# Kernel tuning notes

Hardware: AMD Instinct MI355X
Metric: run time of the kernel (lower is better)

## Reference

```python
import jax, jax.numpy as jnp
import numpy as np

N_NODES = 100000
N_EDGES = 1600000
ATOM_EMB = 64
BOND_EMB = 16
MSG_DIM = 64
OUT_HIDDEN = 128
N_MOLS = 2048
MSG_PASSES = 4


def setup_inputs() -> dict:
    key = jax.random.key(0)
    ks = jax.random.split(key, 16)
    x = jax.random.randint(ks[0], (N_NODES,), 0, 119)
    edge_attr = jax.random.randint(ks[1], (N_EDGES,), 0, 4)
    edge_index = jax.random.randint(ks[2], (2, N_EDGES), 0, N_NODES)
    batch = jnp.sort(jax.random.randint(ks[3], (N_NODES,), 0, N_MOLS))
    s = 0.02
    atom_table = jax.random.normal(ks[4], (119, ATOM_EMB), jnp.float32) * s
    bond_table = jax.random.normal(ks[5], (4, BOND_EMB), jnp.float32) * s
    Wi = jax.random.normal(ks[6], (ATOM_EMB + BOND_EMB, MSG_DIM), jnp.float32) * s
    bi = jnp.zeros((MSG_DIM,), jnp.float32)
    Wu = jax.random.normal(ks[7], (ATOM_EMB + BOND_EMB + MSG_DIM, MSG_DIM), jnp.float32) * s
    bu = jnp.zeros((MSG_DIM,), jnp.float32)
    W1 = jax.random.normal(ks[8], (MSG_DIM, OUT_HIDDEN), jnp.float32) * s
    b1 = jnp.zeros((OUT_HIDDEN,), jnp.float32)
    W2 = jax.random.normal(ks[9], (OUT_HIDDEN, 1), jnp.float32) * s
    b2 = jnp.zeros((1,), jnp.float32)
    return {"x": x, "edge_attr": edge_attr, "edge_index": edge_index, "batch": batch,
            "atom_table": atom_table, "bond_table": bond_table,
            "Wi": Wi, "bi": bi, "Wu": Wu, "bu": bu,
            "W1": W1, "b1": b1, "W2": W2, "b2": b2}


def reference(x, edge_attr, edge_index, batch, atom_table, bond_table, Wi, bi, Wu, bu, W1, b1, W2, b2):
    atom = atom_table[x]                      # [N, ATOM_EMB]
    bond = bond_table[edge_attr]              # [E, BOND_EMB]
    src, dst = edge_index[0], edge_index[1]
    atom_src = atom[src]                      # [E, ATOM_EMB]
    ab = jnp.concatenate([atom_src, bond], axis=1)
    msg = jax.nn.relu(ab @ Wi + bi)           # [E, MSG_DIM]
    for _ in range(MSG_PASSES):
        agg = jax.ops.segment_sum(msg, dst, num_segments=N_NODES)  # [N, MSG_DIM]
        upd_in = jnp.concatenate([ab, agg[src]], axis=1)           # [E, 144]
        msg = jax.nn.relu(upd_in @ Wu + bu)
    node_state = jax.ops.segment_sum(msg, dst, num_segments=N_NODES)
    mol_state = jax.ops.segment_sum(node_state, batch, num_segments=N_MOLS)
    h = jax.nn.relu(mol_state @ W1 + b1)
    return (h @ W2 + b2).squeeze(-1)          # [N_MOLS]
```

## Files before the change

### kernel.cpp

```cpp
#include <hip/hip_runtime.h>

#define MSG 64
#define SLICE_SHIFT 9
#define SLICE_N (1 << SLICE_SHIFT)
#define MAXSLICES 256
#define REP 8
#define CAP_R 1536
#define CAP_E 12288
#define CAP_B 16384
#define NBIN 64

typedef _Float16 h2 __attribute__((ext_vector_type(2)));
typedef _Float16 h4 __attribute__((ext_vector_type(4)));
typedef _Float16 h8 __attribute__((ext_vector_type(8)));

__device__ inline h8 relu8(h8 v) {
    h8 z = {};
    return __builtin_elementwise_max(v, z);
}

__device__ inline h2 u2h(unsigned u) { union { unsigned u; h2 h; } c; c.u = u; return c.h; }

__global__ void setup_kernel(const float* __restrict__ atom, const float* __restrict__ bond,
                             const float* __restrict__ Wi, const float* __restrict__ bi,
                             const float* __restrict__ Wu, const float* __restrict__ bu,
                             const float* __restrict__ Wagg,
                             _Float16* __restrict__ tAi, _Float16* __restrict__ tBi,
                             _Float16* __restrict__ tAu, _Float16* __restrict__ tBu,
                             unsigned* __restrict__ wst, int* __restrict__ gcur,
                             int* __restrict__ bcnt, float* __restrict__ mol,
                             int AR, int K, int ab) {
    int b = blockIdx.x;
    if (b < 2 * ab + 2) {
        bool upd = b >= ab + 1;
        const float* W = upd ? Wu : Wi;
        int lb = upd ? b - (ab + 1) : b;
        if (lb < ab) {
            _Float16* tA = upd ? tAu : tAi;
            int t = lb * 256 + threadIdx.x;
            if (t < AR * MSG) {
                int i = t & 63, a = t >> 6;
                float s = 0.f;
                for (int k = 0; k < 64; ++k) s = fmaf(atom[a * 64 + k], W[k * 64 + i], s);
                tA[t] = (_Float16)s;
            }
        } else {
            _Float16* tBo = upd ? tBu : tBi;
            const float* bias = upd ? bu : bi;
            const float* W16 = W + 64 * MSG;
            int t = threadIdx.x;
            int i = t & 63, r = t >> 6;
            float s = bias[i];
            for (int k = 0; k < 16; ++k) s = fmaf(bond[r * 16 + k], W16[k * 64 + i], s);
            tBo[t] = (_Float16)s;
        }
    } else if (b < 2 * ab + 10) {
        int t = (b - (2 * ab + 2)) * 256 + threadIdx.x;
        if (t < 2048) {
            int k2 = t >> 6, c = t & 63;
            h2 h; h[0] = (_Float16)Wagg[(2 * k2) * 64 + c]; h[1] = (_Float16)Wagg[(2 * k2 + 1) * 64 + c];
            union { h2 h; unsigned u; } cv; cv.h = h;
            wst[k2 * 64 + c] = cv.u;
        }
    } else if (b == 2 * ab + 10) {
        for (int q = threadIdx.x; q < K * REP; q += 256) gcur[q] = q * CAP_R;
        if (threadIdx.x < NBIN) bcnt[threadIdx.x] = 0;
    } else {
        int t = (b - (2 * ab + 11)) * 256 + threadIdx.x;
        ((float4*)mol)[t] = make_float4(0.f, 0.f, 0.f, 0.f);
    }
}

__global__ void node_init_kernel(const int* __restrict__ x, const _Float16* __restrict__ tA,
                                 _Float16* __restrict__ bufC, int N) {
    int t = blockIdx.x * blockDim.x + threadIdx.x;
    int v = t >> 3, j = t & 7;
    if (v < N) ((h8*)bufC)[(long long)v * 8 + j] = ((const h8*)tA)[x[v] * 8 + j];
}

__global__ __launch_bounds__(256) void partition_kernel(
    const int* __restrict__ ei, const int* __restrict__ eattr,
    int E, int* __restrict__ gcur, unsigned long long* __restrict__ aux, int K)
{
    __shared__ int cnt[MAXSLICES];
    __shared__ int lexcl[MAXSLICES];
    __shared__ int gbase[MAXSLICES];
    __shared__ int wsum[4];
    __shared__ unsigned long long stage[1024];
    if (threadIdx.x < MAXSLICES) cnt[threadIdx.x] = 0;
    __syncthreads();
    int rep = blockIdx.x & (REP - 1);
    int e0 = blockIdx.x * 1024;
    int total = min(1024, E - e0);
    int sl[4]; int rk[4]; unsigned long long rec[4];
#pragma unroll
    for (int r = 0; r < 4; ++r) {
        sl[r] = -1;
        int e = e0 + r * 256 + threadIdx.x;
        if (e < E) {
            int s = ei[e], d = ei[E + e];
            rec[r] = ((unsigned long long)((unsigned)s | ((unsigned)eattr[e] << 17)) << 17) | (unsigned)d;
            sl[r] = d >> SLICE_SHIFT;
            rk[r] = atomicAdd(&cnt[sl[r]], 1);
        }
    }
    __syncthreads();
    {
        int c = cnt[threadIdx.x];
        int lane = threadIdx.x & 63, w = threadIdx.x >> 6;
        int sc = c;
        for (int off = 1; off < 64; off <<= 1) { int t = __shfl_up(sc, off); if (lane >= off) sc += t; }
        if (lane == 63) wsum[w] = sc;
        __syncthreads();
        int add = 0;
        for (int q = 0; q < 3; ++q) if (w > q) add += wsum[q];
        lexcl[threadIdx.x] = sc + add - c;
        if (threadIdx.x < K && c > 0)
            gbase[threadIdx.x] = atomicAdd(&gcur[threadIdx.x * REP + rep], c);
    }
    __syncthreads();
#pragma unroll
    for (int r = 0; r < 4; ++r)
        if (sl[r] >= 0) stage[lexcl[sl[r]] + rk[r]] = rec[r];
    __syncthreads();
#pragma unroll
    for (int r = 0; r < 4; ++r) {
        int i = r * 256 + threadIdx.x;
        if (i < total) {
            unsigned long long a = stage[i];
            int s = (int)((unsigned)a & 0x1FFFFu) >> SLICE_SHIFT;
            aux[gbase[s] + (i - lexcl[s])] = a;
        }
    }
}

__global__ __launch_bounds__(1024) void place_kernel(
    const unsigned long long* __restrict__ aux, const int* __restrict__ gcur,
    int* __restrict__ nstart, int* __restrict__ ndeg,
    unsigned* __restrict__ packed, int N)
{
    __shared__ int cnt[SLICE_N];
    __shared__ int wsum[8];
    __shared__ unsigned stage[CAP_E];
    int s = blockIdx.x;
    int lo = s << SLICE_SHIFT;
    if (threadIdx.x < SLICE_N) cnt[threadIdx.x] = 0;
    __syncthreads();
    for (int r = 0; r < REP; ++r) {
        int q = s * REP + r;
        int start = q * CAP_R, end = gcur[q];
        for (int idx = start + threadIdx.x; idx < end; idx += 1024)
            atomicAdd(&cnt[(int)(aux[idx] & 0x1FFFFu) & (SLICE_N - 1)], 1);
    }
    __syncthreads();
    int c = 0, sc = 0;
    if (threadIdx.x < SLICE_N) {
        c = cnt[threadIdx.x];
        int lane = threadIdx.x & 63, w = threadIdx.x >> 6;
        sc = c;
        for (int off = 1; off < 64; off <<= 1) { int t = __shfl_up(sc, off); if (lane >= off) sc += t; }
        if (lane == 63) wsum[w] = sc;
    }
    __syncthreads();
    int totale = 0;
    if (threadIdx.x < SLICE_N) {
        int w = threadIdx.x >> 6;
        int add = 0;
        for (int q = 0; q < 7; ++q) if (w > q) add += wsum[q];
        sc += add;
        int v = lo + threadIdx.x;
        if (v < N) { nstart[v] = s * CAP_E + sc - c; ndeg[v] = c; }
    }
    __syncthreads();
    if (threadIdx.x < SLICE_N) cnt[threadIdx.x] = sc - c;
    __syncthreads();
    for (int r = 0; r < REP; ++r) {
        int q = s * REP + r;
        int start = q * CAP_R, end = gcur[q];
        for (int idx = start + threadIdx.x; idx < end; idx += 1024) {
            unsigned long long a = aux[idx];
            int d = (int)(a & 0x1FFFFu);
            int p = atomicAdd(&cnt[d & (SLICE_N - 1)], 1);
            stage[p] = (unsigned)(a >> 17);
        }
    }
    __syncthreads();
    totale = cnt[SLICE_N - 1];
    for (int i = threadIdx.x; i < totale; i += 1024)
        packed[s * CAP_E + i] = stage[i];
}

__global__ __launch_bounds__(256) void dbin_kernel(const int* __restrict__ ndeg, int N,
                                                   int* __restrict__ bcnt, int* __restrict__ bucket) {
    __shared__ int cnt[NBIN];
    __shared__ int base[NBIN];
    if (threadIdx.x < NBIN) cnt[threadIdx.x] = 0;
    __syncthreads();
    int v = blockIdx.x * 256 + threadIdx.x;
    int b = -1, rk = 0;
    if (v < N) { b = min(ndeg[v], NBIN - 1); rk = atomicAdd(&cnt[b], 1); }
    __syncthreads();
    if (threadIdx.x < NBIN && cnt[threadIdx.x] > 0)
        base[threadIdx.x] = atomicAdd(&bcnt[threadIdx.x], cnt[threadIdx.x]);
    __syncthreads();
    if (b >= 0) bucket[b * CAP_B + base[b] + rk] = v;
}

__global__ void compact_kernel(const int* __restrict__ bucket, const int* __restrict__ bcnt,
                               const int* __restrict__ nstart, const int* __restrict__ ndeg,
                               int2* __restrict__ srt) {
    __shared__ int sbase;
    int b = blockIdx.x;
    if (threadIdx.x == 0) {
        int run = 0;
        for (int i = 0; i < b; ++i) run += bcnt[i];
        sbase = run;
    }
    __syncthreads();
    int n = bcnt[b], base = sbase;
    for (int i = threadIdx.x; i < n; i += 256) {
        int v = bucket[b * CAP_B + i];
        srt[base + i] = make_int2(nstart[v], v | (ndeg[v] << 17));
    }
}

template <bool FINAL>
__global__ __launch_bounds__(256, 8) void gather_kernel(
    const unsigned* __restrict__ packed, const int2* __restrict__ srt,
    const _Float16* __restrict__ nodearr, const _Float16* __restrict__ tB,
    const unsigned* __restrict__ wst_g, const _Float16* __restrict__ tAu,
    const int* __restrict__ x, _Float16* __restrict__ out, int N)
{
    __shared__ _Float16 tbs[4 * 64];
    __shared__ unsigned wst[32 * 64];
    __shared__ _Float16 rowb[32][72];
    tbs[threadIdx.x] = tB[threadIdx.x];
    if (!FINAL)
        for (int idx = threadIdx.x; idx < 2048; idx += 256) wst[idx] = wst_g[idx];
    __syncthreads();
    int t = blockIdx.x * 256 + threadIdx.x;
    int vi = t >> 3;
    int j = threadIdx.x & 7;
    int w = threadIdx.x >> 3;
    const h8* na8 = (const h8*)nodearr;
    const _Float16* tbsj = tbs + j * 8;
    h8 acc = {};
    int v = 0;
    bool valid = vi < N;
    if (valid) {
        int2 s2 = srt[vi];
        int e = s2.x;
        v = (int)((unsigned)s2.y & 0x1FFFFu);
        int end = e + (int)((unsigned)s2.y >> 17);
        for (; e + 7 < end; e += 8) {
            unsigned q0 = packed[e],     q1 = packed[e + 1], q2 = packed[e + 2], q3 = packed[e + 3];
            unsigned q4 = packed[e + 4], q5 = packed[e + 5], q6 = packed[e + 6], q7 = packed[e + 7];
            h8 m0 = na8[(q0 & 0x1FFFFu) * 8 + j];
            h8 m1 = na8[(q1 & 0x1FFFFu) * 8 + j];
            h8 m2 = na8[(q2 & 0x1FFFFu) * 8 + j];
            h8 m3 = na8[(q3 & 0x1FFFFu) * 8 + j];
            h8 m4 = na8[(q4 & 0x1FFFFu) * 8 + j];
            h8 m5 = na8[(q5 & 0x1FFFFu) * 8 + j];
            h8 m6 = na8[(q6 & 0x1FFFFu) * 8 + j];
            h8 m7 = na8[(q7 & 0x1FFFFu) * 8 + j];
            h8 t0 = *(const h8*)&tbsj[(q0 >> 17) * 64];
            h8 t1 = *(const h8*)&tbsj[(q1 >> 17) * 64];
            h8 t2 = *(const h8*)&tbsj[(q2 >> 17) * 64];
            h8 t3 = *(const h8*)&tbsj[(q3 >> 17) * 64];
            h8 t4 = *(const h8*)&tbsj[(q4 >> 17) * 64];
            h8 t5 = *(const h8*)&tbsj[(q5 >> 17) * 64];
            h8 t6 = *(const h8*)&tbsj[(q6 >> 17) * 64];
            h8 t7 = *(const h8*)&tbsj[(q7 >> 17) * 64];
            h8 s0 = relu8(m0 + t0), s1 = relu8(m1 + t1);
            h8 s2v = relu8(m2 + t2), s3 = relu8(m3 + t3);
            h8 s4 = relu8(m4 + t4), s5 = relu8(m5 + t5);
            h8 s6 = relu8(m6 + t6), s7 = relu8(m7 + t7);
            acc += ((s0 + s1) + (s2v + s3)) + ((s4 + s5) + (s6 + s7));
        }
        for (; e < end; ++e) {
            unsigned q0 = packed[e];
            h8 m0 = na8[(q0 & 0x1FFFFu) * 8 + j];
            h8 t0 = *(const h8*)&tbsj[(q0 >> 17) * 64];
            acc += relu8(m0 + t0);
        }
    }
    if (FINAL) {
        if (valid) ((h8*)out)[(long long)v * 8 + j] = acc;
        return;
    }
    *(h8*)&rowb[w][j * 8] = acc;
    __syncthreads();
    if (!valid) return;
    const h2* rp = (const h2*)&rowb[w][0];
    const unsigned* wj = wst + j * 8;
    float o0 = 0.f, o1 = 0.f, o2 = 0.f, o3 = 0.f, o4 = 0.f, o5 = 0.f, o6 = 0.f, o7 = 0.f;
#pragma unroll
    for (int k2 = 0; k2 < 32; ++k2) {
        h2 r = rp[k2];
        uint4 wa = *(const uint4*)&wj[k2 * 64];
        uint4 wb = *(const uint4*)&wj[k2 * 64 + 4];
        o0 = __builtin_amdgcn_fdot2(r, u2h(wa.x), o0, false);
        o1 = __builtin_amdgcn_fdot2(r, u2h(wa.y), o1, false);
        o2 = __builtin_amdgcn_fdot2(r, u2h(wa.z), o2, false);
        o3 = __builtin_amdgcn_fdot2(r, u2h(wa.w), o3, false);
        o4 = __builtin_amdgcn_fdot2(r, u2h(wb.x), o4, false);
        o5 = __builtin_amdgcn_fdot2(r, u2h(wb.y), o5, false);
        o6 = __builtin_amdgcn_fdot2(r, u2h(wb.z), o6, false);
        o7 = __builtin_amdgcn_fdot2(r, u2h(wb.w), o7, false);
    }
    h8 ta = ((const h8*)tAu)[x[v] * 8 + j];
    h8 o;
    o[0] = (_Float16)(o0 + (float)ta[0]); o[1] = (_Float16)(o1 + (float)ta[1]);
    o[2] = (_Float16)(o2 + (float)ta[2]); o[3] = (_Float16)(o3 + (float)ta[3]);
    o[4] = (_Float16)(o4 + (float)ta[4]); o[5] = (_Float16)(o5 + (float)ta[5]);
    o[6] = (_Float16)(o6 + (float)ta[6]); o[7] = (_Float16)(o7 + (float)ta[7]);
    ((h8*)out)[(long long)v * 8 + j] = o;
}

__global__ void mol_pool_kernel(const _Float16* __restrict__ ns, const int* __restrict__ batch,
                                float* __restrict__ mol, int N) {
    int g = (blockIdx.x * blockDim.x + threadIdx.x) >> 4;
    int j = threadIdx.x & 15;
    int n0 = g * 32;
    if (n0 >= N) return;
    int n1 = min(n0 + 32, N);
    const h4* ns4 = (const h4*)ns;
    int cur = batch[n0];
    float ax = 0.f, ay = 0.f, az = 0.f, aw = 0.f;
    for (int n = n0; n < n1; ++n) {
        int b = batch[n];
        if (b != cur) {
            float* mp = &mol[(long long)cur * 64 + j * 4];
            atomicAdd(mp + 0, ax); atomicAdd(mp + 1, ay);
            atomicAdd(mp + 2, az); atomicAdd(mp + 3, aw);
            ax = ay = az = aw = 0.f; cur = b;
        }
        h4 vv = ns4[(long long)n * 16 + j];
        ax += (float)vv.x; ay += (float)vv.y; az += (float)vv.z; aw += (float)vv.w;
    }
    float* mp = &mol[(long long)cur * 64 + j * 4];
    atomicAdd(mp + 0, ax); atomicAdd(mp + 1, ay);
    atomicAdd(mp + 2, az); atomicAdd(mp + 3, aw);
}

__global__ void head_kernel(const float* __restrict__ mol, const float* __restrict__ W1,
                            const float* __restrict__ b1, const float* __restrict__ W2,
                            const float* __restrict__ b2, float* __restrict__ out) {
    int g = blockIdx.x;
    int j = threadIdx.x;
    float s = b1[j];
#pragma unroll
    for (int k = 0; k < 64; ++k) s = fmaf(mol[g * 64 + k], W1[k * 128 + j], s);
    s = fmaxf(s, 0.0f) * W2[j];
    __shared__ float red[128];
    red[j] = s;
    __syncthreads();
    for (int off = 64; off > 0; off >>= 1) {
        if (j < off) red[j] += red[j + off];
        __syncthreads();
    }
    if (j == 0) out[g] = red[0] + b2[0];
}

extern "C" void kernel_launch(void* const* d_in, const int* in_sizes, int n_in,
                              void* d_out, int out_size, void* d_ws, size_t ws_size,
                              hipStream_t stream) {
    const int*   x          = (const int*)d_in[0];
    const int*   eattr      = (const int*)d_in[1];
    const int*   ei         = (const int*)d_in[2];
    const int*   batch      = (const int*)d_in[3];
    const float* atom_table = (const float*)d_in[4];
    const float* bond_table = (const float*)d_in[5];
    const float* Wi         = (const float*)d_in[6];
    const float* bi         = (const float*)d_in[7];
    const float* Wu         = (const float*)d_in[8];
    const float* bu         = (const float*)d_in[9];
    const float* W1         = (const float*)d_in[10];
    const float* b1         = (const float*)d_in[11];
    const float* W2         = (const float*)d_in[12];
    const float* b2         = (const float*)d_in[13];

    const int N = in_sizes[0];
    const int E = in_sizes[1];
    const int M = out_size;
    const int AR = in_sizes[4] / 64;
    const int K = (N + SLICE_N - 1) >> SLICE_SHIFT;
    const int ab = (AR * MSG + 255) / 256;

    char* ws = (char*)d_ws;
    size_t off_b = 0;
    auto alloc = [&](size_t bytes) -> void* {
        void* p = ws + off_b;
        off_b = (off_b + bytes + 255) & ~(size_t)255;
        return p;
    };
    size_t nbytes = (size_t)N * MSG * 2;
    size_t abytes = (size_t)K * REP * CAP_R * 8;
    _Float16* bufA  = (_Float16*)alloc(nbytes);
    _Float16* bufB  = (_Float16*)alloc(nbytes > abytes ? nbytes : abytes);
    _Float16* bufC  = (_Float16*)alloc(nbytes);
    unsigned long long* aux = (unsigned long long*)bufB;
    unsigned* packed = (unsigned*)alloc((size_t)K * CAP_E * 4);
    int*      nstart = (int*)alloc((size_t)N * 4);
    int*      ndeg   = (int*)alloc((size_t)N * 4);
    int2*     srt    = (int2*)alloc((size_t)N * 8);
    int*      bucket = (int*)alloc((size_t)NBIN * CAP_B * 4);
    int*      bcnt   = (int*)alloc((size_t)NBIN * 4);
    int*      gcur   = (int*)alloc((size_t)K * REP * 4);
    _Float16* tAi    = (_Float16*)alloc((size_t)AR * MSG * 2);
    _Float16* tBi    = (_Float16*)alloc((size_t)4 * MSG * 2);
    _Float16* tAu    = (_Float16*)alloc((size_t)AR * MSG * 2);
    _Float16* tBu    = (_Float16*)alloc((size_t)4 * MSG * 2);
    unsigned* wstb   = (unsigned*)alloc((size_t)32 * 64 * 4);
    float*    mol    = (float*)alloc((size_t)M * MSG * 4);
    (void)ws_size; (void)n_in;

    const float* Wagg = Wu + 80 * MSG;

    setup_kernel<<<2 * ab + 11 + 128, 256, 0, stream>>>(atom_table, bond_table, Wi, bi, Wu, bu, Wagg,
                                                        tAi, tBi, tAu, tBu, wstb, gcur, bcnt, mol,
                                                        AR, K, ab);
    node_init_kernel<<<(int)(((long long)N * 8 + 255) / 256), 256, 0, stream>>>(x, tAi, bufC, N);

    partition_kernel<<<(E + 1023) / 1024, 256, 0, stream>>>(ei, eattr, E, gcur, aux, K);
    place_kernel<<<K, 1024, 0, stream>>>(aux, gcur, nstart, ndeg, packed, N);

    dbin_kernel<<<(N + 255) / 256, 256, 0, stream>>>(ndeg, N, bcnt, bucket);
    compact_kernel<<<NBIN, 256, 0, stream>>>(bucket, bcnt, nstart, ndeg, srt);

    const int gblocks = (int)(((long long)N * 8 + 255) / 256);
    gather_kernel<false><<<gblocks, 256, 0, stream>>>(packed, srt, bufC, tBi, wstb, tAu, x, bufA, N);
    gather_kernel<false><<<gblocks, 256, 0, stream>>>(packed, srt, bufA, tBu, wstb, tAu, x, bufB, N);
    gather_kernel<false><<<gblocks, 256, 0, stream>>>(packed, srt, bufB, tBu, wstb, tAu, x, bufA, N);
    gather_kernel<false><<<gblocks, 256, 0, stream>>>(packed, srt, bufA, tBu, wstb, tAu, x, bufB, N);
    gather_kernel<true><<<gblocks, 256, 0, stream>>>(packed, srt, bufB, tBu, nullptr, nullptr, nullptr, bufA, N);

    mol_pool_kernel<<<(((N + 31) / 32) * 16 + 255) / 256, 256, 0, stream>>>(bufA, batch, mol, N);
    head_kernel<<<M, 128, 0, stream>>>(mol, W1, b1, W2, b2, (float*)d_out);
}
```

Before: 287.0 us.

## Fuse degree binning into place kernel and gather atom embeddings directly in first pass

Degree binning moves into place_kernel, which writes bucket entries with the degree packed into the high bits. This removes dbin_kernel, the ndeg array and the ndeg lookups in compact_kernel. node_init_kernel is also removed: the first gather pass reads the atom table through x[src] instead of a materialised per-node buffer. The cost is two kernel launches and one node-buffer write/read saved, traded for an extra dependent x load per edge in the first gather pass and extra shared-memory atomics in place_kernel.

```diff
diff --git a/kernel.cpp b/kernel.cpp
--- a/kernel.cpp
+++ b/kernel.cpp
@@ -71,13 +71,6 @@
     }
 }
 
-__global__ void node_init_kernel(const int* __restrict__ x, const _Float16* __restrict__ tA,
-                                 _Float16* __restrict__ bufC, int N) {
-    int t = blockIdx.x * blockDim.x + threadIdx.x;
-    int v = t >> 3, j = t & 7;
-    if (v < N) ((h8*)bufC)[(long long)v * 8 + j] = ((const h8*)tA)[x[v] * 8 + j];
-}
-
 __global__ __launch_bounds__(256) void partition_kernel(
     const int* __restrict__ ei, const int* __restrict__ eattr,
     int E, int* __restrict__ gcur, unsigned long long* __restrict__ aux, int K)
@@ -136,15 +129,18 @@
 
 __global__ __launch_bounds__(1024) void place_kernel(
     const unsigned long long* __restrict__ aux, const int* __restrict__ gcur,
-    int* __restrict__ nstart, int* __restrict__ ndeg,
+    int* __restrict__ nstart, int* __restrict__ bcnt, int* __restrict__ bucket,
     unsigned* __restrict__ packed, int N)
 {
     __shared__ int cnt[SLICE_N];
     __shared__ int wsum[8];
     __shared__ unsigned stage[CAP_E];
+    __shared__ int bc[NBIN];
+    __shared__ int bb[NBIN];
     int s = blockIdx.x;
     int lo = s << SLICE_SHIFT;
     if (threadIdx.x < SLICE_N) cnt[threadIdx.x] = 0;
+    if (threadIdx.x >= SLICE_N && threadIdx.x < SLICE_N + NBIN) bc[threadIdx.x - SLICE_N] = 0;
     __syncthreads();
     for (int r = 0; r < REP; ++r) {
         int q = s * REP + r;
@@ -162,16 +158,24 @@
         if (lane == 63) wsum[w] = sc;
     }
     __syncthreads();
-    int totale = 0;
+    int v = lo + threadIdx.x;
+    int bin = -1, rk = 0;
     if (threadIdx.x < SLICE_N) {
         int w = threadIdx.x >> 6;
         int add = 0;
         for (int q = 0; q < 7; ++q) if (w > q) add += wsum[q];
         sc += add;
-        int v = lo + threadIdx.x;
-        if (v < N) { nstart[v] = s * CAP_E + sc - c; ndeg[v] = c; }
-    }
-    __syncthreads();
+        if (v < N) {
+            nstart[v] = s * CAP_E + sc - c;
+            bin = min(c, NBIN - 1);
+            rk = atomicAdd(&bc[bin], 1);
+        }
+    }
+    __syncthreads();
+    if (threadIdx.x < NBIN && bc[threadIdx.x] > 0)
+        bb[threadIdx.x] = atomicAdd(&bcnt[threadIdx.x], bc[threadIdx.x]);
+    __syncthreads();
+    if (bin >= 0) bucket[bin * CAP_B + bb[bin] + rk] = v | (c << 17);
     if (threadIdx.x < SLICE_N) cnt[threadIdx.x] = sc - c;
     __syncthreads();
     for (int r = 0; r < REP; ++r) {
@@ -185,30 +189,13 @@
         }
     }
     __syncthreads();
-    totale = cnt[SLICE_N - 1];
+    int totale = cnt[SLICE_N - 1];
     for (int i = threadIdx.x; i < totale; i += 1024)
         packed[s * CAP_E + i] = stage[i];
 }
 
-__global__ __launch_bounds__(256) void dbin_kernel(const int* __restrict__ ndeg, int N,
-                                                   int* __restrict__ bcnt, int* __restrict__ bucket) {
-    __shared__ int cnt[NBIN];
-    __shared__ int base[NBIN];
-    if (threadIdx.x < NBIN) cnt[threadIdx.x] = 0;
-    __syncthreads();
-    int v = blockIdx.x * 256 + threadIdx.x;
-    int b = -1, rk = 0;
-    if (v < N) { b = min(ndeg[v], NBIN - 1); rk = atomicAdd(&cnt[b], 1); }
-    __syncthreads();
-    if (threadIdx.x < NBIN && cnt[threadIdx.x] > 0)
-        base[threadIdx.x] = atomicAdd(&bcnt[threadIdx.x], cnt[threadIdx.x]);
-    __syncthreads();
-    if (b >= 0) bucket[b * CAP_B + base[b] + rk] = v;
-}
-
 __global__ void compact_kernel(const int* __restrict__ bucket, const int* __restrict__ bcnt,
-                               const int* __restrict__ nstart, const int* __restrict__ ndeg,
-                               int2* __restrict__ srt) {
+                               const int* __restrict__ nstart, int2* __restrict__ srt) {
     __shared__ int sbase;
     int b = blockIdx.x;
     if (threadIdx.x == 0) {
@@ -219,23 +206,25 @@
     __syncthreads();
     int n = bcnt[b], base = sbase;
     for (int i = threadIdx.x; i < n; i += 256) {
-        int v = bucket[b * CAP_B + i];
-        srt[base + i] = make_int2(nstart[v], v | (ndeg[v] << 17));
-    }
-}
-
-template <bool FINAL>
+        int e = bucket[b * CAP_B + i];
+        int v = e & 0x1FFFF;
+        srt[base + i] = make_int2(nstart[v], e);
+    }
+}
+
+template <int MODE>
 __global__ __launch_bounds__(256, 8) void gather_kernel(
     const unsigned* __restrict__ packed, const int2* __restrict__ srt,
     const _Float16* __restrict__ nodearr, const _Float16* __restrict__ tB,
     const unsigned* __restrict__ wst_g, const _Float16* __restrict__ tAu,
-    const int* __restrict__ x, _Float16* __restrict__ out, int N)
+    const int* __restrict__ x, const _Float16* __restrict__ tAi,
+    _Float16* __restrict__ out, int N)
 {
     __shared__ _Float16 tbs[4 * 64];
     __shared__ unsigned wst[32 * 64];
     __shared__ _Float16 rowb[32][72];
     tbs[threadIdx.x] = tB[threadIdx.x];
-    if (!FINAL)
+    if (MODE != 2)
         for (int idx = threadIdx.x; idx < 2048; idx += 256) wst[idx] = wst_g[idx];
     __syncthreads();
     int t = blockIdx.x * 256 + threadIdx.x;
@@ -243,6 +232,7 @@
     int j = threadIdx.x & 7;
     int w = threadIdx.x >> 3;
     const h8* na8 = (const h8*)nodearr;
+    const h8* tAi8 = (const h8*)tAi;
     const _Float16* tbsj = tbs + j * 8;
     h8 acc = {};
     int v = 0;
@@ -255,14 +245,26 @@
         for (; e + 7 < end; e += 8) {
             unsigned q0 = packed[e],     q1 = packed[e + 1], q2 = packed[e + 2], q3 = packed[e + 3];
             unsigned q4 = packed[e + 4], q5 = packed[e + 5], q6 = packed[e + 6], q7 = packed[e + 7];
-            h8 m0 = na8[(q0 & 0x1FFFFu) * 8 + j];
-            h8 m1 = na8[(q1 & 0x1FFFFu) * 8 + j];
-            h8 m2 = na8[(q2 & 0x1FFFFu) * 8 + j];
-            h8 m3 = na8[(q3 & 0x1FFFFu) * 8 + j];
-            h8 m4 = na8[(q4 & 0x1FFFFu) * 8 + j];
-            h8 m5 = na8[(q5 & 0x1FFFFu) * 8 + j];
-            h8 m6 = na8[(q6 & 0x1FFFFu) * 8 + j];
-            h8 m7 = na8[(q7 & 0x1FFFFu) * 8 + j];
+            h8 m0, m1, m2, m3, m4, m5, m6, m7;
+            if (MODE == 0) {
+                m0 = tAi8[(long long)x[q0 & 0x1FFFFu] * 8 + j];
+                m1 = tAi8[(long long)x[q1 & 0x1FFFFu] * 8 + j];
+                m2 = tAi8[(long long)x[q2 & 0x1FFFFu] * 8 + j];
+                m3 = tAi8[(long long)x[q3 & 0x1FFFFu] * 8 + j];
+                m4 = tAi8[(long long)x[q4 & 0x1FFFFu] * 8 + j];
+                m5 = tAi8[(long long)x[q5 & 0x1FFFFu] * 8 + j];
+                m6 = tAi8[(long long)x[q6 & 0x1FFFFu] * 8 + j];
+                m7 = tAi8[(long long)x[q7 & 0x1FFFFu] * 8 + j];
+            } else {
+                m0 = na8[(q0 & 0x1FFFFu) * 8 + j];
+                m1 = na8[(q1 & 0x1FFFFu) * 8 + j];
+                m2 = na8[(q2 & 0x1FFFFu) * 8 + j];
+                m3 = na8[(q3 & 0x1FFFFu) * 8 + j];
+                m4 = na8[(q4 & 0x1FFFFu) * 8 + j];
+                m5 = na8[(q5 & 0x1FFFFu) * 8 + j];
+                m6 = na8[(q6 & 0x1FFFFu) * 8 + j];
+                m7 = na8[(q7 & 0x1FFFFu) * 8 + j];
+            }
             h8 t0 = *(const h8*)&tbsj[(q0 >> 17) * 64];
             h8 t1 = *(const h8*)&tbsj[(q1 >> 17) * 64];
             h8 t2 = *(const h8*)&tbsj[(q2 >> 17) * 64];
@@ -279,12 +281,14 @@
         }
         for (; e < end; ++e) {
             unsigned q0 = packed[e];
-            h8 m0 = na8[(q0 & 0x1FFFFu) * 8 + j];
+            h8 m0;
+            if (MODE == 0) m0 = tAi8[(long long)x[q0 & 0x1FFFFu] * 8 + j];
+            else           m0 = na8[(q0 & 0x1FFFFu) * 8 + j];
             h8 t0 = *(const h8*)&tbsj[(q0 >> 17) * 64];
             acc += relu8(m0 + t0);
         }
     }
-    if (FINAL) {
+    if (MODE == 2) {
         if (valid) ((h8*)out)[(long long)v * 8 + j] = acc;
         return;
     }
@@ -398,11 +402,9 @@
     size_t abytes = (size_t)K * REP * CAP_R * 8;
     _Float16* bufA  = (_Float16*)alloc(nbytes);
     _Float16* bufB  = (_Float16*)alloc(nbytes > abytes ? nbytes : abytes);
-    _Float16* bufC  = (_Float16*)alloc(nbytes);
     unsigned long long* aux = (unsigned long long*)bufB;
     unsigned* packed = (unsigned*)alloc((size_t)K * CAP_E * 4);
     int*      nstart = (int*)alloc((size_t)N * 4);
-    int*      ndeg   = (int*)alloc((size_t)N * 4);
     int2*     srt    = (int2*)alloc((size_t)N * 8);
     int*      bucket = (int*)alloc((size_t)NBIN * CAP_B * 4);
     int*      bcnt   = (int*)alloc((size_t)NBIN * 4);
@@ -420,20 +422,17 @@
     setup_kernel<<<2 * ab + 11 + 128, 256, 0, stream>>>(atom_table, bond_table, Wi, bi, Wu, bu, Wagg,
                                                         tAi, tBi, tAu, tBu, wstb, gcur, bcnt, mol,
                                                         AR, K, ab);
-    node_init_kernel<<<(int)(((long long)N * 8 + 255) / 256), 256, 0, stream>>>(x, tAi, bufC, N);
 
     partition_kernel<<<(E + 1023) / 1024, 256, 0, stream>>>(ei, eattr, E, gcur, aux, K);
-    place_kernel<<<K, 1024, 0, stream>>>(aux, gcur, nstart, ndeg, packed, N);
-
-    dbin_kernel<<<(N + 255) / 256, 256, 0, stream>>>(ndeg, N, bcnt, bucket);
-    compact_kernel<<<NBIN, 256, 0, stream>>>(bucket, bcnt, nstart, ndeg, srt);
+    place_kernel<<<K, 1024, 0, stream>>>(aux, gcur, nstart, bcnt, bucket, packed, N);
+    compact_kernel<<<NBIN, 256, 0, stream>>>(bucket, bcnt, nstart, srt);
 
     const int gblocks = (int)(((long long)N * 8 + 255) / 256);
-    gather_kernel<false><<<gblocks, 256, 0, stream>>>(packed, srt, bufC, tBi, wstb, tAu, x, bufA, N);
-    gather_kernel<false><<<gblocks, 256, 0, stream>>>(packed, srt, bufA, tBu, wstb, tAu, x, bufB, N);
-    gather_kernel<false><<<gblocks, 256, 0, stream>>>(packed, srt, bufB, tBu, wstb, tAu, x, bufA, N);
-    gather_kernel<false><<<gblocks, 256, 0, stream>>>(packed, srt, bufA, tBu, wstb, tAu, x, bufB, N);
-    gather_kernel<true><<<gblocks, 256, 0, stream>>>(packed, srt, bufB, tBu, nullptr, nullptr, nullptr, bufA, N);
+    gather_kernel<0><<<gblocks, 256, 0, stream>>>(packed, srt, nullptr, tBi, wstb, tAu, x, tAi, bufA, N);
+    gather_kernel<1><<<gblocks, 256, 0, stream>>>(packed, srt, bufA, tBu, wstb, tAu, x, nullptr, bufB, N);
+    gather_kernel<1><<<gblocks, 256, 0, stream>>>(packed, srt, bufB, tBu, wstb, tAu, x, nullptr, bufA, N);
+    gather_kernel<1><<<gblocks, 256, 0, stream>>>(packed, srt, bufA, tBu, wstb, tAu, x, nullptr, bufB, N);
+    gather_kernel<2><<<gblocks, 256, 0, stream>>>(packed, srt, bufB, tBu, nullptr, nullptr, nullptr, nullptr, bufA, N);
 
     mol_pool_kernel<<<(((N + 31) / 32) * 16 + 255) / 256, 256, 0, stream>>>(bufA, batch, mol, N);
     head_kernel<<<M, 128, 0, stream>>>(mol, W1, b1, W2, b2, (float*)d_out);
```

Measured after the change: 264.4 us. -7.9%, faster.
